# Kernel optimization log

Hardware: AMD Instinct MI355X
Metric: run time of the kernel (lower is better)

## Reference

```python
import jax, jax.numpy as jnp
import numpy as np

BATCH, PAST_N, HID, FEAT = 256, 512, 512, 1
INIT_MULT = 0.01  # ones * 0.01 initial state (perturb_init=False / eval mode)


def setup_inputs() -> dict:
    key = jax.random.key(0)
    ks = jax.random.split(key, 8)
    s = 1.0 / np.sqrt(HID)
    return {
        "input_seq": jax.random.normal(ks[0], (BATCH, PAST_N, FEAT), dtype=jnp.float32),
        "future_n": 64,
        "W_ih": jax.random.uniform(ks[1], (4 * HID, FEAT), minval=-s, maxval=s, dtype=jnp.float32),
        "W_hh": jax.random.uniform(ks[2], (4 * HID, HID), minval=-s, maxval=s, dtype=jnp.float32),
        "b_ih": jax.random.uniform(ks[3], (4 * HID,), minval=-s, maxval=s, dtype=jnp.float32),
        "b_hh": jax.random.uniform(ks[4], (4 * HID,), minval=-s, maxval=s, dtype=jnp.float32),
        "W_dec": jax.random.uniform(ks[5], (FEAT, HID), minval=-s, maxval=s, dtype=jnp.float32),
        "b_dec": jax.random.uniform(ks[6], (FEAT,), minval=-s, maxval=s, dtype=jnp.float32),
    }


def _lstm_cell(x, h, c, W_ih, W_hh, b_ih, b_hh):
    # PyTorch LSTMCell: gates ordered (i, f, g, o)
    gates = x @ W_ih.T + b_ih + h @ W_hh.T + b_hh  # [B, 4H]
    i, f, g, o = jnp.split(gates, 4, axis=-1)
    c_new = jax.nn.sigmoid(f) * c + jax.nn.sigmoid(i) * jnp.tanh(g)
    h_new = jax.nn.sigmoid(o) * jnp.tanh(c_new)
    return h_new, c_new


def reference(input_seq, future_n, W_ih, W_hh, b_ih, b_hh, W_dec, b_dec):
    B, T, _ = input_seq.shape
    h0 = jnp.full((B, HID), INIT_MULT, dtype=input_seq.dtype)
    c0 = jnp.full((B, HID), INIT_MULT, dtype=input_seq.dtype)

    xs = jnp.swapaxes(input_seq, 0, 1)  # [T, B, F]

    def past_step(carry, x_t):
        h, c = carry
        h, c = _lstm_cell(x_t, h, c, W_ih, W_hh, b_ih, b_hh)
        return (h, c), h

    (h, c), past_h = jax.lax.scan(past_step, (h0, c0), xs)  # past_h: [T, B, H]

    def future_step(carry, _):
        h, c = carry
        x_t = h @ W_dec.T + b_dec  # decode hidden -> next input, [B, F]
        h, c = _lstm_cell(x_t, h, c, W_ih, W_hh, b_ih, b_hh)
        return (h, c), h

    _, fut_h = jax.lax.scan(future_step, (h, c), None, length=future_n)  # [F_n, B, H]

    all_h = jnp.concatenate([past_h, fut_h], axis=0)  # [T+F_n, B, H]
    all_h = jnp.swapaxes(all_h, 0, 1)  # [B, T+F_n, H]
    return all_h @ W_dec.T + b_dec  # [B, T+F_n, 1]
```

## Files before the change

### kernel.cpp

```cpp
#include <hip/hip_runtime.h>
#include <hip/hip_fp16.h>


#define TPAST 512
#define TTOT  576
#define HIDN  512
#define BW    16
#define HW    64
#define NWG   128
#define NTHR  512
#define HSTR  520
#define GSTR  261
#define BATCHN 256

typedef _Float16 half8   __attribute__((ext_vector_type(8)));
typedef _Float16 half2v  __attribute__((ext_vector_type(2)));
typedef float    float4v __attribute__((ext_vector_type(4)));
typedef int      int4v   __attribute__((ext_vector_type(4)));

__device__ __forceinline__ float fast_exp(float x) {
    return __builtin_amdgcn_exp2f(x * 1.44269504f);
}
__device__ __forceinline__ float fast_sigmoid(float x) {
    return __builtin_amdgcn_rcpf(1.0f + fast_exp(-x));
}
__device__ __forceinline__ float fast_tanh(float x) {
    return 1.0f - 2.0f * __builtin_amdgcn_rcpf(fast_exp(2.0f * x) + 1.0f);
}

__device__ __forceinline__ void ld32_agent(const void* p, int4v& a, int4v& b) {
    asm volatile("global_load_dwordx4 %0, %2, off sc1\n\t"
                 "global_load_dwordx4 %1, %2, off offset:16 sc1\n\t"
                 "s_waitcnt vmcnt(0)"
                 : "=v"(a), "=v"(b) : "v"(p) : "memory");
}
__device__ __forceinline__ void drain_vm() {
    asm volatile("s_waitcnt vmcnt(0)" ::: "memory");
}

__global__ __launch_bounds__(NTHR, 1)
void lstm_forecast_kernel(const float* __restrict__ xseq,
                          const float* __restrict__ Wih,
                          const float* __restrict__ Whh,
                          const float* __restrict__ bih,
                          const float* __restrict__ bhh,
                          const float* __restrict__ Wdec,
                          const float* __restrict__ bdec,
                          float* __restrict__ out,
                          unsigned int* __restrict__ flagbase,
                          unsigned int* __restrict__ hbuf)
{
    __shared__ _Float16 hcur[BW * HSTR];
    __shared__ float    gates[BW * GSTR];
    __shared__ float    wdecs[HIDN];
    __shared__ float    xcur[BW];

    const int tid  = threadIdx.x;
    const int bb   = blockIdx.x & 15;
    const int gb   = blockIdx.x >> 4;
    const int lane = tid & 63;
    const int wave = tid >> 6;
    const int m    = lane & 15;
    const int q    = lane >> 4;

    half8 Wf[2][16];
    {
        #pragma unroll
        for (int cbi = 0; cbi < 2; ++cbi) {
            const int col = (2 * wave + cbi) * 16 + m;
            const int gt  = col >> 6;
            const int jl  = col & 63;
            const float* wr = Whh + (size_t)(gt * HIDN + gb * HW + jl) * HIDN;
            #pragma unroll
            for (int kk = 0; kk < 16; ++kk) {
                const int k0 = kk * 32 + q * 8;
                float4v u = *(const float4v*)(wr + k0);
                float4v v = *(const float4v*)(wr + k0 + 4);
                half8 h;
                h[0] = (_Float16)u[0]; h[1] = (_Float16)u[1];
                h[2] = (_Float16)u[2]; h[3] = (_Float16)u[3];
                h[4] = (_Float16)v[0]; h[5] = (_Float16)v[1];
                h[6] = (_Float16)v[2]; h[7] = (_Float16)v[3];
                Wf[cbi][kk] = h;
            }
        }
    }

    const int eb = tid >> 5;
    const int jj = tid & 31;
    const int j0 = 2 * jj;
    float wih_r[2][4], bsum_r[2][4];
    #pragma unroll
    for (int p = 0; p < 2; ++p) {
        const int jg = gb * HW + j0 + p;
        #pragma unroll
        for (int gt = 0; gt < 4; ++gt) {
            const int r = gt * HIDN + jg;
            wih_r[p][gt]  = Wih[r];
            bsum_r[p][gt] = bih[r] + bhh[r];
        }
    }
    const float bdecv = bdec[0];
    float c0 = 0.01f, c1 = 0.01f;

    {
        const _Float16 hinit = (_Float16)0.01f;
        for (int i = tid; i < BW * HSTR; i += NTHR) hcur[i] = hinit;
        wdecs[tid] = Wdec[tid];
        if (tid < BW) xcur[tid] = xseq[(bb * BW + tid) * TPAST + 0];
    }
    __syncthreads();

    unsigned int* flag_own =
        flagbase + (size_t)(((bb << 3) | gb) << 3 | wave) * 16;
    const unsigned int* poll_slot =
        flagbase + (size_t)(((bb << 3) | wave) << 3 | (lane & 7)) * 16;
    const int bglob_e = bb * BW + eb;

    for (int t = 0; t < TTOT; ++t) {
        float4v acc0 = {0.f, 0.f, 0.f, 0.f};
        float4v acc1 = {0.f, 0.f, 0.f, 0.f};
        const _Float16* arow = hcur + m * HSTR + q * 8;
        #pragma unroll
        for (int kk = 0; kk < 16; ++kk) {
            half8 af = *(const half8*)(arow + kk * 32);
            acc0 = __builtin_amdgcn_mfma_f32_16x16x32_f16(af, Wf[0][kk], acc0, 0, 0, 0);
            acc1 = __builtin_amdgcn_mfma_f32_16x16x32_f16(af, Wf[1][kk], acc1, 0, 0, 0);
        }
        {
            const int colbase = wave * 32;
            #pragma unroll
            for (int r = 0; r < 4; ++r) {
                gates[(q * 4 + r) * GSTR + colbase +      m] = acc0[r];
                gates[(q * 4 + r) * GSTR + colbase + 16 + m] = acc1[r];
            }
        }
        const int tn = t + 1;
        float xq = 0.f;
        if (tn < TPAST && tid < BW) xq = xseq[(bb * BW + tid) * TPAST + tn];

        __syncthreads();

        {
            const float xc = xcur[eb];
            const float* grow = gates + eb * GSTR;

            float gi = grow[       j0] + xc * wih_r[0][0] + bsum_r[0][0];
            float gf = grow[ 64  + j0] + xc * wih_r[0][1] + bsum_r[0][1];
            float gg = grow[128  + j0] + xc * wih_r[0][2] + bsum_r[0][2];
            float go = grow[192  + j0] + xc * wih_r[0][3] + bsum_r[0][3];
            c0 = fast_sigmoid(gf) * c0 + fast_sigmoid(gi) * fast_tanh(gg);
            const float h0 = fast_sigmoid(go) * fast_tanh(c0);

            gi = grow[       j0 + 1] + xc * wih_r[1][0] + bsum_r[1][0];
            gf = grow[ 64  + j0 + 1] + xc * wih_r[1][1] + bsum_r[1][1];
            gg = grow[128  + j0 + 1] + xc * wih_r[1][2] + bsum_r[1][2];
            go = grow[192  + j0 + 1] + xc * wih_r[1][3] + bsum_r[1][3];
            c1 = fast_sigmoid(gf) * c1 + fast_sigmoid(gi) * fast_tanh(gg);
            const float h1 = fast_sigmoid(go) * fast_tanh(c1);

            half2v hp; hp[0] = (_Float16)h0; hp[1] = (_Float16)h1;

            *(half2v*)(hcur + eb * HSTR + gb * HW + j0) = hp;

            const unsigned int bits = __builtin_bit_cast(unsigned int, hp);
            unsigned int* hdst = hbuf
                + (size_t)((tn & 1) * BATCHN + bglob_e) * (HIDN / 2)
                + gb * (HW / 2) + jj;
            __hip_atomic_store(hdst, bits, __ATOMIC_RELAXED,
                               __HIP_MEMORY_SCOPE_AGENT);
        }

        const unsigned int target = (unsigned int)tn;
        drain_vm();
        if (lane == 0)
            __hip_atomic_store(flag_own, target, __ATOMIC_RELAXED,
                               __HIP_MEMORY_SCOPE_AGENT);

        if (wave != gb) {
            int guard = 0;
            for (;;) {
                const unsigned int v = __hip_atomic_load(
                    poll_slot, __ATOMIC_RELAXED, __HIP_MEMORY_SCOPE_AGENT);
                if (__ballot(v >= target) == ~0ull) break;
                __builtin_amdgcn_s_sleep(1);
                if (++guard > (1 << 20)) break;
            }
            __builtin_amdgcn_sched_barrier(0);

            const int p1 = tn & 1;
            const char* src = (const char*)hbuf
                + ((size_t)(p1 * BATCHN + bb * BW)) * (HIDN * 2)
                + (size_t)(lane >> 2) * (HIDN * 2)
                + wave * (HW * 2)
                + (lane & 3) * 32;
            int4v a, b;
            ld32_agent(src, a, b);
            _Float16* dst = hcur + (lane >> 2) * HSTR + wave * HW
                            + (lane & 3) * 16;
            *(int4v*)(dst)     = a;
            *(int4v*)(dst + 8) = b;
        }
        __syncthreads();

        if (wave < 2) {
            const int brow = 2 * gb + wave;
            const _Float16* hr = hcur + brow * HSTR + lane * 8;
            const float*    wr = wdecs + lane * 8;
            half8 hv = *(const half8*)hr;
            float dx = 0.f;
            #pragma unroll
            for (int e = 0; e < 8; ++e) dx += (float)hv[e] * wr[e];
            dx += __shfl_down(dx, 32);
            dx += __shfl_down(dx, 16);
            dx += __shfl_down(dx, 8);
            dx += __shfl_down(dx, 4);
            dx += __shfl_down(dx, 2);
            dx += __shfl_down(dx, 1);
            if (lane == 0)
                out[(bb * BW + brow) * TTOT + t] = dx + bdecv;
        }
        if (tn >= TPAST) {
            const _Float16* hr = hcur + eb * HSTR + jj * 16;
            const float*    wr = wdecs + jj * 16;
            float dx = 0.f;
            #pragma unroll
            for (int u = 0; u < 2; ++u) {
                half8 hv = *(const half8*)(hr + u * 8);
                #pragma unroll
                for (int e = 0; e < 8; ++e)
                    dx += (float)hv[e] * wr[u * 8 + e];
            }
            dx += __shfl_down(dx, 16);
            dx += __shfl_down(dx, 8);
            dx += __shfl_down(dx, 4);
            dx += __shfl_down(dx, 2);
            dx += __shfl_down(dx, 1);
            if ((lane & 31) == 0) xcur[eb] = dx + bdecv;
        } else {
            if (tid < BW) xcur[tid] = xq;
        }
    }
}

extern "C" void kernel_launch(void* const* d_in, const int* in_sizes, int n_in,
                              void* d_out, int out_size, void* d_ws, size_t ws_size,
                              hipStream_t stream) {
    (void)in_sizes; (void)n_in; (void)ws_size; (void)out_size;
    const float* xseq = (const float*)d_in[0];
    const float* Wih  = (const float*)d_in[2];
    const float* Whh  = (const float*)d_in[3];
    const float* bih  = (const float*)d_in[4];
    const float* bhh  = (const float*)d_in[5];
    const float* Wdec = (const float*)d_in[6];
    const float* bdec = (const float*)d_in[7];
    float* out = (float*)d_out;

    unsigned int* flags = (unsigned int*)d_ws;
    unsigned int* hbuf  = (unsigned int*)((char*)d_ws + 65536);

    hipMemsetAsync(d_ws, 0, 65536, stream);
    lstm_forecast_kernel<<<dim3(NWG), dim3(NTHR), 0, stream>>>(
        xseq, Wih, Whh, bih, bhh, Wdec, bdec, out, flags, hbuf);
}
```

Before: 1.800 ms.

## Replace flag-based inter-workgroup sync with tag bits embedded in hidden-state data

Removes the separate per-wave flag array and the vmcnt drain before the flag store. The step-parity tag now lives in the low mantissa bit of each packed fp16 pair in the exchange buffer, and consumers poll and validate the data words directly. This cuts one global store and its drain from every step, along with the store-to-flag-to-data round trip. In exchange it costs one mantissa bit of h precision, adds a retry loop on the data load, and relies on 0x00/0xFF initialisation of the two parity buffers.

```diff
diff --git a/kernel.cpp b/kernel.cpp
--- a/kernel.cpp
+++ b/kernel.cpp
@@ -34,9 +34,6 @@
                  "s_waitcnt vmcnt(0)"
                  : "=v"(a), "=v"(b) : "v"(p) : "memory");
 }
-__device__ __forceinline__ void drain_vm() {
-    asm volatile("s_waitcnt vmcnt(0)" ::: "memory");
-}
 
 __global__ __launch_bounds__(NTHR, 1)
 void lstm_forecast_kernel(const float* __restrict__ xseq,
@@ -47,7 +44,6 @@
                           const float* __restrict__ Wdec,
                           const float* __restrict__ bdec,
                           float* __restrict__ out,
-                          unsigned int* __restrict__ flagbase,
                           unsigned int* __restrict__ hbuf)
 {
     __shared__ _Float16 hcur[BW * HSTR];
@@ -111,10 +107,6 @@
     }
     __syncthreads();
 
-    unsigned int* flag_own =
-        flagbase + (size_t)(((bb << 3) | gb) << 3 | wave) * 16;
-    const unsigned int* poll_slot =
-        flagbase + (size_t)(((bb << 3) | wave) << 3 | (lane & 7)) * 16;
     const int bglob_e = bb * BW + eb;
 
     for (int t = 0; t < TTOT; ++t) {
@@ -136,6 +128,7 @@
             }
         }
         const int tn = t + 1;
+        const unsigned int tag = ((unsigned int)tn >> 1) & 1u;
         float xq = 0.f;
         if (tn < TPAST && tid < BW) xq = xseq[(bb * BW + tid) * TPAST + tn];
 
@@ -163,7 +156,8 @@
 
             *(half2v*)(hcur + eb * HSTR + gb * HW + j0) = hp;
 
-            const unsigned int bits = __builtin_bit_cast(unsigned int, hp);
+            unsigned int bits = __builtin_bit_cast(unsigned int, hp);
+            bits = (bits & ~1u) | tag;
             unsigned int* hdst = hbuf
                 + (size_t)((tn & 1) * BATCHN + bglob_e) * (HIDN / 2)
                 + gb * (HW / 2) + jj;
@@ -171,24 +165,21 @@
                                __HIP_MEMORY_SCOPE_AGENT);
         }
 
-        const unsigned int target = (unsigned int)tn;
-        drain_vm();
-        if (lane == 0)
-            __hip_atomic_store(flag_own, target, __ATOMIC_RELAXED,
-                               __HIP_MEMORY_SCOPE_AGENT);
-
         if (wave != gb) {
+            const int p1 = tn & 1;
+            const unsigned int* prow0 = hbuf
+                + (size_t)(p1 * BATCHN + bb * BW + (lane & 15)) * (HIDN / 2)
+                + wave * (HW / 2);
             int guard = 0;
             for (;;) {
                 const unsigned int v = __hip_atomic_load(
-                    poll_slot, __ATOMIC_RELAXED, __HIP_MEMORY_SCOPE_AGENT);
-                if (__ballot(v >= target) == ~0ull) break;
+                    prow0, __ATOMIC_RELAXED, __HIP_MEMORY_SCOPE_AGENT);
+                if (__ballot(((v ^ tag) & 1u) == 0u) == ~0ull) break;
                 __builtin_amdgcn_s_sleep(1);
                 if (++guard > (1 << 20)) break;
             }
             __builtin_amdgcn_sched_barrier(0);
 
-            const int p1 = tn & 1;
             const char* src = (const char*)hbuf
                 + ((size_t)(p1 * BATCHN + bb * BW)) * (HIDN * 2)
                 + (size_t)(lane >> 2) * (HIDN * 2)
@@ -196,6 +187,17 @@
                 + (lane & 3) * 32;
             int4v a, b;
             ld32_agent(src, a, b);
+            for (;;) {
+                const unsigned int av = a[0] & a[1] & a[2] & a[3]
+                                      & b[0] & b[1] & b[2] & b[3];
+                const unsigned int ov = a[0] | a[1] | a[2] | a[3]
+                                      | b[0] | b[1] | b[2] | b[3];
+                const bool ok = tag ? ((av & 1u) != 0u) : ((ov & 1u) == 0u);
+                if (__ballot(ok) == ~0ull) break;
+                __builtin_amdgcn_s_sleep(1);
+                if (++guard > (1 << 20)) break;
+                ld32_agent(src, a, b);
+            }
             _Float16* dst = hcur + (lane >> 2) * HSTR + wave * HW
                             + (lane & 3) * 16;
             *(int4v*)(dst)     = a;
@@ -256,10 +258,11 @@
     const float* bdec = (const float*)d_in[7];
     float* out = (float*)d_out;
 
-    unsigned int* flags = (unsigned int*)d_ws;
-    unsigned int* hbuf  = (unsigned int*)((char*)d_ws + 65536);
-
-    hipMemsetAsync(d_ws, 0, 65536, stream);
+    unsigned int* hbuf = (unsigned int*)d_ws;
+    const size_t half_bytes = (size_t)BATCHN * HIDN * 2;
+
+    hipMemsetAsync(hbuf, 0x00, half_bytes, stream);
+    hipMemsetAsync((char*)hbuf + half_bytes, 0xFF, half_bytes, stream);
     lstm_forecast_kernel<<<dim3(NWG), dim3(NTHR), 0, stream>>>(
-        xseq, Wih, Whh, bih, bhh, Wdec, bdec, out, flags, hbuf);
-}
+        xseq, Wih, Whh, bih, bhh, Wdec, bdec, out, hbuf);
+}
```

Measured after the change: 1.763 ms. 1.02x faster.
